# Optimization experiments

Hardware: AMD Instinct MI355X
Metric: run time of the kernel (lower is better)

Reference implementation:

```python
import jax, jax.numpy as jnp
import numpy as np

N, E, F, H, C, G = 100000, 1600000, 128, 4, 32, 64
D = H * C  # 128, per-layer node dim
NEG_SLOPE = 0.2
BN_EPS = 1e-5


def setup_inputs() -> dict:
    key = jax.random.key(0)
    ks = jax.random.split(key, 24)
    inp = {
        "x": jax.random.normal(ks[0], (N, F), jnp.float32),
        "edge_index": jax.random.randint(ks[1], (2, E), 0, N, jnp.int64),
        "batch": jnp.sort(jax.random.randint(ks[2], (N,), 0, G, jnp.int64)),
        # GATConv layer 0: in=F, out=C per head
        "w0": jax.random.normal(ks[3], (F, H * C), jnp.float32) * 0.1,
        "att_src0": jax.random.normal(ks[4], (H, C), jnp.float32) * 0.1,
        "att_dst0": jax.random.normal(ks[5], (H, C), jnp.float32) * 0.1,
        "bias0": jax.random.normal(ks[6], (H * C,), jnp.float32) * 0.1,
        # GATConv layer 1: in=D, out=C per head
        "w1": jax.random.normal(ks[7], (D, H * C), jnp.float32) * 0.1,
        "att_src1": jax.random.normal(ks[8], (H, C), jnp.float32) * 0.1,
        "att_dst1": jax.random.normal(ks[9], (H, C), jnp.float32) * 0.1,
        "bias1": jax.random.normal(ks[10], (H * C,), jnp.float32) * 0.1,
        # BatchNorm (eval mode: running stats)
        "bn_g0": jax.random.normal(ks[11], (D,), jnp.float32) * 0.1 + 1.0,
        "bn_b0": jax.random.normal(ks[12], (D,), jnp.float32) * 0.1,
        "bn_m0": jax.random.normal(ks[13], (D,), jnp.float32) * 0.1,
        "bn_v0": jax.random.uniform(ks[14], (D,), jnp.float32) + 0.5,
        "bn_g1": jax.random.normal(ks[15], (D,), jnp.float32) * 0.1 + 1.0,
        "bn_b1": jax.random.normal(ks[16], (D,), jnp.float32) * 0.1,
        "bn_m1": jax.random.normal(ks[17], (D,), jnp.float32) * 0.1,
        "bn_v1": jax.random.uniform(ks[18], (D,), jnp.float32) + 0.5,
        # head MLP
        "lin1_w": jax.random.normal(ks[19], (D, D // 2), jnp.float32) * 0.1,
        "lin1_b": jax.random.normal(ks[20], (D // 2,), jnp.float32) * 0.1,
        "lin2_w": jax.random.normal(ks[21], (D // 2, 1), jnp.float32) * 0.1,
        "lin2_b": jax.random.normal(ks[22], (1,), jnp.float32) * 0.1,
    }
    return inp


def gat_conv(x, src, dst, w, att_s, att_d, bias):
    """PyG GATConv (concat=True, add_self_loops already in src/dst), eval mode."""
    n = x.shape[0]
    h = (x @ w).reshape(n, H, C)                       # [N,H,C]
    a_s = jnp.sum(h * att_s, axis=-1)                   # [N,H]
    a_d = jnp.sum(h * att_d, axis=-1)                   # [N,H]
    e = jax.nn.leaky_relu(a_s[src] + a_d[dst], NEG_SLOPE)  # [Etot,H]
    m = jax.ops.segment_max(e, dst, num_segments=n)
    m = jax.lax.stop_gradient(jnp.where(jnp.isfinite(m), m, 0.0))
    ex = jnp.exp(e - m[dst])
    denom = jax.ops.segment_sum(ex, dst, num_segments=n)
    alpha = ex / (denom[dst] + 1e-16)                    # segment softmax over dst
    out = jax.ops.segment_sum(h[src] * alpha[:, :, None], dst, num_segments=n)
    return out.reshape(n, H * C) + bias


def bn_eval(x, g, b, m, v):
    return (x - m) * jax.lax.rsqrt(v + BN_EPS) * g + b


def reference(x, edge_index, batch,
              w0, att_src0, att_dst0, bias0,
              w1, att_src1, att_dst1, bias1,
              bn_g0, bn_b0, bn_m0, bn_v0,
              bn_g1, bn_b1, bn_m1, bn_v1,
              lin1_w, lin1_b, lin2_w, lin2_b):
    n = x.shape[0]
    loops = jnp.arange(n, dtype=edge_index.dtype)
    src = jnp.concatenate([edge_index[0], loops])
    dst = jnp.concatenate([edge_index[1], loops])

    h = gat_conv(x, src, dst, w0, att_src0, att_dst0, bias0)
    h = jax.nn.relu(bn_eval(h, bn_g0, bn_b0, bn_m0, bn_v0))
    h = gat_conv(h, src, dst, w1, att_src1, att_dst1, bias1)
    h = jax.nn.relu(bn_eval(h, bn_g1, bn_b1, bn_m1, bn_v1))

    # global mean pool over graphs
    summed = jax.ops.segment_sum(h, batch, num_segments=G)           # [G,D]
    counts = jax.ops.segment_sum(jnp.ones((n,), h.dtype), batch, num_segments=G)
    pooled = summed / jnp.maximum(counts, 1.0)[:, None]

    z = jax.nn.relu(pooled @ lin1_w + lin1_b)
    return z @ lin2_w + lin2_b                                        # [G,1]
```

## Files before the change

### kernel.cpp

```cpp
#include <hip/hip_runtime.h>

#define GG 64
#define STRIDE 10240
#define NBINMAX 256

typedef __attribute__((ext_vector_type(8))) short short8;
typedef __attribute__((ext_vector_type(4))) float f32x4;


__device__ inline unsigned short bf16rne(float f) {
  unsigned int x = __float_as_uint(f);
  unsigned int r = (x + 0x7FFFu + ((x >> 16) & 1u)) >> 16;
  return (unsigned short)r;
}
__device__ inline unsigned int pack2(float a, float b) {
  return (unsigned int)bf16rne(a) | ((unsigned int)bf16rne(b) << 16);
}
__device__ inline float blo(unsigned int v) { return __uint_as_float(v << 16); }
__device__ inline float bhi(unsigned int v) { return __uint_as_float(v & 0xFFFF0000u); }


__global__ __launch_bounds__(256) void init_gcur(int* __restrict__ gcur) {
  gcur[threadIdx.x] = threadIdx.x * STRIDE;
}

__global__ __launch_bounds__(256) void part_p1(const int* __restrict__ ei,
                                               int* __restrict__ gcur,
                                               unsigned int* __restrict__ pairs,
                                               int E, int N) {
  __shared__ int hist[NBINMAX];
  __shared__ int gbase[NBINMAX];
  __shared__ int lcur[NBINMAX];
  int t = threadIdx.x;
  int tot = E + N;
  int base = blockIdx.x * 4096;
  hist[t] = 0;
  __syncthreads();
  int sarr[16], darr[16];
  #pragma unroll
  for (int k = 0; k < 16; ++k) {
    int i = base + k * 256 + t;
    if (i < tot) {
      int s, d;
      if (i < E) { s = ei[i]; d = ei[E + i]; } else { s = i - E; d = s; }
      sarr[k] = s; darr[k] = d;
      atomicAdd(&hist[d >> 9], 1);
    } else darr[k] = -1;
  }
  __syncthreads();
  int c = hist[t];
  gbase[t] = (c > 0) ? atomicAdd(&gcur[t], c) : 0;
  lcur[t] = 0;
  __syncthreads();
  #pragma unroll
  for (int k = 0; k < 16; ++k) {
    int d = darr[k];
    if (d >= 0) {
      int b = d >> 9;
      int p = gbase[b] + atomicAdd(&lcur[b], 1);
      pairs[p] = ((unsigned int)(d & 511) << 17) | (unsigned int)sarr[k];
    }
  }
}


__global__ __launch_bounds__(256) void part_p2(const unsigned int* __restrict__ pairs,
                                               const int* __restrict__ gcur,
                                               int* __restrict__ ssrc,
                                               int* __restrict__ offsets,
                                               int* __restrict__ counts, int N) {
  __shared__ int ncnt[512], ncur[512], excl_s[512];
  __shared__ int wsum[4];
  int b = blockIdx.x;
  int t = threadIdx.x;
  int pb = b * STRIDE;
  int cnt = gcur[b] - pb;
  ncnt[t] = 0; ncnt[t + 256] = 0;
  __syncthreads();
  for (int e = t; e < cnt; e += 256) {
    unsigned int v = pairs[pb + e];
    atomicAdd(&ncnt[v >> 17], 1);
  }
  __syncthreads();
  int c0 = ncnt[2 * t], c1 = ncnt[2 * t + 1];
  int ps = c0 + c1;
  int lane = t & 63, w = t >> 6;
  int x = ps;
  #pragma unroll
  for (int s = 1; s < 64; s <<= 1) { int y = __shfl_up(x, s); if (lane >= s) x += y; }
  if (lane == 63) wsum[w] = x;
  __syncthreads();
  int woff = 0;
  for (int i = 0; i < w; ++i) woff += wsum[i];
  int ep = woff + x - ps;
  excl_s[2 * t]     = ep;
  excl_s[2 * t + 1] = ep + c0;
  __syncthreads();
  int binstart = b << 9;
  for (int i = t; i < 512; i += 256) {
    ncur[i] = excl_s[i];
    int node = binstart + i;
    if (node < N) { offsets[node] = pb + excl_s[i]; counts[node] = ncnt[i]; }
  }
  __syncthreads();
  for (int e = t; e < cnt; e += 256) {
    unsigned int v = pairs[pb + e];
    int dl = v >> 17;
    int p = atomicAdd(&ncur[dl], 1);
    ssrc[pb + p] = (int)(v & 0x1FFFF);
  }
}


__global__ __launch_bounds__(256) void gbounds(const int* __restrict__ batch,
                                               int* __restrict__ gstart, int N) {
  int i = blockIdx.x * 256 + threadIdx.x;
  if (i >= N) return;
  int g = batch[i];
  if (i == 0 || batch[i - 1] != g) gstart[g] = i;
}

__global__ void gfix(const int* __restrict__ gstart, int* __restrict__ go,
                     int* __restrict__ ge, int N) {
  if (threadIdx.x == 0 && blockIdx.x == 0) {
    int nxt = N;
    for (int g = GG - 1; g >= 0; --g) {
      int s = gstart[g];
      if (s < 0) { go[g] = nxt; ge[g] = nxt; }
      else       { go[g] = s;   ge[g] = nxt; nxt = s; }
    }
  }
}


__global__ __launch_bounds__(256) void wprep(const float* __restrict__ w0,
                                             const float* __restrict__ w1,
                                             unsigned short* __restrict__ wt) {
  int idx = blockIdx.x * 256 + threadIdx.x;
  int layer = idx >> 14;
  int e = idx & 16383;
  int k = e >> 7, n = e & 127;
  float v = (layer ? w1 : w0)[e];
  unsigned short hi = bf16rne(v);
  float hif = __uint_as_float((unsigned int)hi << 16);
  unsigned short lo = bf16rne(v - hif);
  unsigned short* basep = wt + layer * 32768;
  basep[n * 128 + k] = hi;
  basep[16384 + n * 128 + k] = lo;
}


__global__ __launch_bounds__(256) void gemm_mfma(
    const float* __restrict__ in, const unsigned short* __restrict__ wtL,
    const float* __restrict__ att_s, const float* __restrict__ att_d,
    unsigned int* __restrict__ h16, float* __restrict__ a_s,
    float* __restrict__ a_d, int N) {
  __shared__ unsigned short xh[128][40], xl[128][40];
  int t = threadIdx.x;
  int bid = blockIdx.x;
  int ch = bid & 1;
  int base = (bid >> 1) * 128;
  int lane = t & 63, w = t >> 6;
  int l15 = lane & 15, lg = lane >> 4;
  int hd = w & 1;
  int n0 = ch * 64 + hd * 32;
  int rh = w >> 1;

  f32x4 zero4 = {0.f, 0.f, 0.f, 0.f};
  f32x4 acc[4][2];
  #pragma unroll
  for (int rt = 0; rt < 4; ++rt) { acc[rt][0] = zero4; acc[rt][1] = zero4; }

  int sr = t >> 1;
  int sc = (t & 1) * 16;
  int gr = base + sr;
  int rc = gr < N ? gr : (N - 1);
  const float* xp = &in[(size_t)rc * 128 + sc];

  const unsigned short* wh0 = &wtL[(size_t)(n0 + l15) * 128];
  const unsigned short* wh1 = &wtL[(size_t)(n0 + 16 + l15) * 128];

  float4 u0 = *(const float4*)(xp + 0);
  float4 u1 = *(const float4*)(xp + 4);
  float4 u2 = *(const float4*)(xp + 8);
  float4 u3 = *(const float4*)(xp + 12);
  short8 cbh0 = *(const short8*)(wh0 + lg * 8);
  short8 cbh1 = *(const short8*)(wh1 + lg * 8);
  short8 cbl0 = *(const short8*)(wh0 + 16384 + lg * 8);
  short8 cbl1 = *(const short8*)(wh1 + 16384 + lg * 8);

  #pragma unroll
  for (int kt = 0; kt < 4; ++kt) {
    if (kt) __syncthreads();
    {
      float4 uu[4] = {u0, u1, u2, u3};
      #pragma unroll
      for (int q = 0; q < 4; ++q) {
        float4 u = uu[q];
        unsigned int b0 = __float_as_uint(u.x), b1 = __float_as_uint(u.y);
        unsigned int b2 = __float_as_uint(u.z), b3 = __float_as_uint(u.w);
        *(unsigned int*)&xh[sr][sc + q * 4]     = __builtin_amdgcn_perm(b1, b0, 0x07060302u);
        *(unsigned int*)&xh[sr][sc + q * 4 + 2] = __builtin_amdgcn_perm(b3, b2, 0x07060302u);
        float r0 = u.x - __uint_as_float(b0 & 0xFFFF0000u);
        float r1 = u.y - __uint_as_float(b1 & 0xFFFF0000u);
        float r2 = u.z - __uint_as_float(b2 & 0xFFFF0000u);
        float r3 = u.w - __uint_as_float(b3 & 0xFFFF0000u);
        *(unsigned int*)&xl[sr][sc + q * 4] =
            __builtin_amdgcn_perm(__float_as_uint(r1), __float_as_uint(r0), 0x07060302u);
        *(unsigned int*)&xl[sr][sc + q * 4 + 2] =
            __builtin_amdgcn_perm(__float_as_uint(r3), __float_as_uint(r2), 0x07060302u);
      }
    }
    __syncthreads();
    float4 v0 = u0, v1 = u1, v2 = u2, v3 = u3;
    short8 nbh0 = cbh0, nbh1 = cbh1, nbl0 = cbl0, nbl1 = cbl1;
    if (kt < 3) {
      int k1 = (kt + 1) * 32;
      v0 = *(const float4*)(xp + k1);
      v1 = *(const float4*)(xp + k1 + 4);
      v2 = *(const float4*)(xp + k1 + 8);
      v3 = *(const float4*)(xp + k1 + 12);
      nbh0 = *(const short8*)(wh0 + k1 + lg * 8);
      nbh1 = *(const short8*)(wh1 + k1 + lg * 8);
      nbl0 = *(const short8*)(wh0 + 16384 + k1 + lg * 8);
      nbl1 = *(const short8*)(wh1 + 16384 + k1 + lg * 8);
    }
    #pragma unroll
    for (int rt = 0; rt < 4; ++rt) {
      int row = rh * 64 + rt * 16 + l15;
      short8 fah = *(const short8*)&xh[row][lg * 8];
      short8 fal = *(const short8*)&xl[row][lg * 8];
      acc[rt][0] = __builtin_amdgcn_mfma_f32_16x16x32_bf16(fah, cbh0, acc[rt][0], 0, 0, 0);
      acc[rt][1] = __builtin_amdgcn_mfma_f32_16x16x32_bf16(fah, cbh1, acc[rt][1], 0, 0, 0);
      acc[rt][0] = __builtin_amdgcn_mfma_f32_16x16x32_bf16(fal, cbh0, acc[rt][0], 0, 0, 0);
      acc[rt][1] = __builtin_amdgcn_mfma_f32_16x16x32_bf16(fal, cbh1, acc[rt][1], 0, 0, 0);
      acc[rt][0] = __builtin_amdgcn_mfma_f32_16x16x32_bf16(fah, cbl0, acc[rt][0], 0, 0, 0);
      acc[rt][1] = __builtin_amdgcn_mfma_f32_16x16x32_bf16(fah, cbl1, acc[rt][1], 0, 0, 0);
    }
    u0 = v0; u1 = v1; u2 = v2; u3 = v3;
    cbh0 = nbh0; cbh1 = nbh1; cbl0 = nbl0; cbl1 = nbl1;
  }

  int headg = ch * 2 + hd;
  float as0 = att_s[n0 + l15], as1 = att_s[n0 + 16 + l15];
  float ad0 = att_d[n0 + l15], ad1 = att_d[n0 + 16 + l15];
  #pragma unroll
  for (int rt = 0; rt < 4; ++rt) {
    float ps[4], pd[4];
    #pragma unroll
    for (int q = 0; q < 4; ++q) {
      float c0v = acc[rt][0][q], c1v = acc[rt][1][q];
      float p0 = __shfl_xor(c0v, 1), p1 = __shfl_xor(c1v, 1);
      int row = base + rh * 64 + rt * 16 + lg * 4 + q;
      if (!(l15 & 1) && row < N) {
        h16[(size_t)row * 64 + (n0 + l15) / 2]      = pack2(c0v, p0);
        h16[(size_t)row * 64 + (n0 + 16 + l15) / 2] = pack2(c1v, p1);
      }
      ps[q] = c0v * as0 + c1v * as1;
      pd[q] = c0v * ad0 + c1v * ad1;
    }
    #pragma unroll
    for (int m = 1; m <= 8; m <<= 1) {
      #pragma unroll
      for (int q = 0; q < 4; ++q) { ps[q] += __shfl_xor(ps[q], m); pd[q] += __shfl_xor(pd[q], m); }
    }
    if (l15 == 0) {
      #pragma unroll
      for (int q = 0; q < 4; ++q) {
        int row = base + rh * 64 + rt * 16 + lg * 4 + q;
        if (row < N) { a_s[row * 4 + headg] = ps[q]; a_d[row * 4 + headg] = pd[q]; }
      }
    }
  }
}


#define ACCP(EX, V0, V1)                                                       \
  { float2 ex2 = make_float2(EX, EX);                                          \
    acc2[0] += ex2 * make_float2(blo(V0.x), bhi(V0.x));                        \
    acc2[1] += ex2 * make_float2(blo(V0.y), bhi(V0.y));                        \
    acc2[2] += ex2 * make_float2(blo(V0.z), bhi(V0.z));                        \
    acc2[3] += ex2 * make_float2(blo(V0.w), bhi(V0.w));                        \
    acc2[4] += ex2 * make_float2(blo(V1.x), bhi(V1.x));                        \
    acc2[5] += ex2 * make_float2(blo(V1.y), bhi(V1.y));                        \
    acc2[6] += ex2 * make_float2(blo(V1.z), bhi(V1.z));                        \
    acc2[7] += ex2 * make_float2(blo(V1.w), bhi(V1.w)); }

__global__ __launch_bounds__(256) void gat_aggregate(
    const unsigned int* __restrict__ h16, const float* __restrict__ a_s, const float* __restrict__ a_d,
    const int* __restrict__ offsets, const int* __restrict__ counts, const int* __restrict__ ssrc,
    const float* __restrict__ bias,
    const float* __restrict__ bn_g, const float* __restrict__ bn_b,
    const float* __restrict__ bn_m, const float* __restrict__ bn_v,
    float* __restrict__ out, int N) {
  __shared__ float part[4][8][132];
  int wv = threadIdx.x >> 6;
  int lane = threadIdx.x & 63;
  int wid = blockIdx.x * 4 + wv;
  if (wid >= N) return;
  int off = offsets[wid], cnt = counts[wid];
  int eg = lane >> 3;
  int j  = lane & 7;
  int hh = j >> 1;
  float ad = a_d[wid * 4 + hh];

  float2 acc2[8] = {};
  float den = 0.f;

  int sA = ssrc[off + (eg < cnt ? eg : 0)];
  int iB0 = eg + 8;
  int sB = ssrc[off + (iB0 < cnt ? iB0 : 0)];
  float asA = a_s[sA * 4 + hh];
  float asB = a_s[sB * 4 + hh];

  for (int i = eg; i < cnt; i += 16) {
    const uint4* hpA = (const uint4*)(h16 + (size_t)sA * 64 + j * 8);
    uint4 va0 = hpA[0], va1 = hpA[1];
    const uint4* hpB = (const uint4*)(h16 + (size_t)sB * 64 + j * 8);
    uint4 vb0 = hpB[0], vb1 = hpB[1];
    int in0 = i + 16, in1 = i + 24;
    int snA = ssrc[off + (in0 < cnt ? in0 : 0)];
    int snB = ssrc[off + (in1 < cnt ? in1 : 0)];
    float anA = a_s[snA * 4 + hh];
    float anB = a_s[snB * 4 + hh];
    float eA = asA + ad; eA = eA > 0.f ? eA : 0.2f * eA;
    float exA = __expf(eA);
    float eB = asB + ad; eB = eB > 0.f ? eB : 0.2f * eB;
    float exB = ((i + 8) < cnt) ? __expf(eB) : 0.f;
    den += exA + exB;
    ACCP(exA, va0, va1)
    ACCP(exB, vb0, vb1)
    sA = snA; sB = snB; asA = anA; asB = anB;
  }

  den += __shfl_xor(den, 8);
  den += __shfl_xor(den, 16);
  den += __shfl_xor(den, 32);
  den = __shfl(den, (lane >> 4) * 2);

  float* pw = &part[wv][eg][j * 16];
  *(float4*)(pw + 0)  = make_float4(acc2[0].x, acc2[0].y, acc2[1].x, acc2[1].y);
  *(float4*)(pw + 4)  = make_float4(acc2[2].x, acc2[2].y, acc2[3].x, acc2[3].y);
  *(float4*)(pw + 8)  = make_float4(acc2[4].x, acc2[4].y, acc2[5].x, acc2[5].y);
  *(float4*)(pw + 12) = make_float4(acc2[6].x, acc2[6].y, acc2[7].x, acc2[7].y);
  asm volatile("s_waitcnt lgkmcnt(0)" ::: "memory");

  int d = lane * 2;
  float r0 = 0.f, r1 = 0.f;
  #pragma unroll
  for (int g = 0; g < 8; ++g) {
    float2 v = *(const float2*)(&part[wv][g][d]);
    r0 += v.x; r1 += v.y;
  }

  float inv = 1.f / (den + 1e-16f);
  float2 bi = *(const float2*)(&bias[d]);
  float2 g2 = *(const float2*)(&bn_g[d]);
  float2 b2 = *(const float2*)(&bn_b[d]);
  float2 m2 = *(const float2*)(&bn_m[d]);
  float2 v2 = *(const float2*)(&bn_v[d]);
  float o0 = r0 * inv + bi.x;
  float o1 = r1 * inv + bi.y;
  o0 = fmaxf((o0 - m2.x) * (g2.x * rsqrtf(v2.x + 1e-5f)) + b2.x, 0.f);
  o1 = fmaxf((o1 - m2.y) * (g2.y * rsqrtf(v2.y + 1e-5f)) + b2.y, 0.f);
  *(float2*)(&out[(size_t)wid * 128 + d]) = make_float2(o0, o1);
}


#define POOLP 8

__global__ __launch_bounds__(256) void pool_kernel(const float* __restrict__ y,
                                                   const int* __restrict__ go,
                                                   const int* __restrict__ ge,
                                                   float* __restrict__ pooled) {
  int g = blockIdx.x / POOLP, p = blockIdx.x % POOLP;
  int s = go[g], e = ge[g];
  int len = e - s;
  int q0 = s + (len * p) / POOLP, q1 = s + (len * (p + 1)) / POOLP;
  int t = threadIdx.x;
  int d = t & 127, half = t >> 7;
  float acc = 0.f;
  for (int i = q0 + half; i < q1; i += 2) acc += y[(size_t)i * 128 + d];
  __shared__ float red[256];
  red[t] = acc;
  __syncthreads();
  if (half == 0) atomicAdd(&pooled[g * 128 + d], red[d] + red[d + 128]);
}

__global__ __launch_bounds__(64) void mlp_kernel(const float* __restrict__ pooled,
                                                 const int* __restrict__ go,
                                                 const int* __restrict__ ge,
                                                 const float* __restrict__ w1,
                                                 const float* __restrict__ b1,
                                                 const float* __restrict__ w2,
                                                 const float* __restrict__ b2,
                                                 float* __restrict__ out) {
  int g = blockIdx.x, j = threadIdx.x;
  int cnt = ge[g] - go[g];
  float inv = 1.f / (float)(cnt > 1 ? cnt : 1);
  float z = b1[j];
  for (int k = 0; k < 128; ++k) z += pooled[g * 128 + k] * inv * w1[k * 64 + j];
  z = fmaxf(z, 0.f);
  float v = z * w2[j];
  #pragma unroll
  for (int m = 1; m < 64; m <<= 1) v += __shfl_xor(v, m);
  if (j == 0) out[g] = v + b2[0];
}


extern "C" void kernel_launch(void* const* d_in, const int* in_sizes, int n_in,
                              void* d_out, int out_size, void* d_ws, size_t ws_size,
                              hipStream_t stream) {
  const float* x     = (const float*)d_in[0];
  const int*   ei    = (const int*)d_in[1];
  const int*   batch = (const int*)d_in[2];
  const float* w0    = (const float*)d_in[3];
  const float* atts0 = (const float*)d_in[4];
  const float* attd0 = (const float*)d_in[5];
  const float* bias0 = (const float*)d_in[6];
  const float* w1    = (const float*)d_in[7];
  const float* atts1 = (const float*)d_in[8];
  const float* attd1 = (const float*)d_in[9];
  const float* bias1 = (const float*)d_in[10];
  const float* bng0  = (const float*)d_in[11];
  const float* bnb0  = (const float*)d_in[12];
  const float* bnm0  = (const float*)d_in[13];
  const float* bnv0  = (const float*)d_in[14];
  const float* bng1  = (const float*)d_in[15];
  const float* bnb1  = (const float*)d_in[16];
  const float* bnm1  = (const float*)d_in[17];
  const float* bnv1  = (const float*)d_in[18];
  const float* l1w   = (const float*)d_in[19];
  const float* l1b   = (const float*)d_in[20];
  const float* l2w   = (const float*)d_in[21];
  const float* l2b   = (const float*)d_in[22];

  int N = in_sizes[2];
  int E = in_sizes[1] / 2;
  int tot = E + N;
  int NBIN = (N + 511) / 512;

  char* p = (char*)d_ws;
  unsigned int* h16 = (unsigned int*)p; p += (size_t)N * 128 * 2;
  float* y_buf  = (float*)p; p += (size_t)N * 128 * 4;
  float* a_s    = (float*)p; p += (size_t)N * 4 * 4;
  float* a_d    = (float*)p; p += (size_t)N * 4 * 4;
  int* counts   = (int*)p;   p += (size_t)N * 4;
  int* offsets  = (int*)p;   p += (size_t)N * 4;
  int* ssrc     = (int*)p;   p += (size_t)NBINMAX * STRIDE * 4;
  int* gcur     = (int*)p;   p += NBINMAX * 4;
  int* gstart   = (int*)p;   p += 64 * 4;
  int* go       = (int*)p;   p += 64 * 4;
  int* ge       = (int*)p;   p += 64 * 4;
  float* pooled = (float*)p; p += 64 * 128 * 4;
  unsigned short* wt = (unsigned short*)p; p += 2 * 32768 * 2;
  unsigned int* pairs = (unsigned int*)y_buf;

  hipMemsetAsync(gstart, 0xFF, 64 * 4, stream);
  hipMemsetAsync(pooled, 0, 64 * 128 * 4, stream);

  int bN = (N + 255) / 256;
  int bW = (N + 3) / 4;
  int bG2 = 2 * ((N + 127) / 128);

  init_gcur<<<1, 256, 0, stream>>>(gcur);
  part_p1<<<(tot + 4095) / 4096, 256, 0, stream>>>(ei, gcur, pairs, E, N);
  part_p2<<<NBIN, 256, 0, stream>>>(pairs, gcur, ssrc, offsets, counts, N);
  gbounds<<<bN, 256, 0, stream>>>(batch, gstart, N);
  gfix<<<1, 64, 0, stream>>>(gstart, go, ge, N);
  wprep<<<128, 256, 0, stream>>>(w0, w1, wt);

  gemm_mfma<<<bG2, 256, 0, stream>>>(x, wt, atts0, attd0, h16, a_s, a_d, N);
  gat_aggregate<<<bW, 256, 0, stream>>>(h16, a_s, a_d, offsets, counts, ssrc,
                                        bias0, bng0, bnb0, bnm0, bnv0, y_buf, N);
  gemm_mfma<<<bG2, 256, 0, stream>>>(y_buf, wt + 32768, atts1, attd1, h16, a_s, a_d, N);
  gat_aggregate<<<bW, 256, 0, stream>>>(h16, a_s, a_d, offsets, counts, ssrc,
                                        bias1, bng1, bnb1, bnm1, bnv1, y_buf, N);
  pool_kernel<<<GG * POOLP, 256, 0, stream>>>(y_buf, go, ge, pooled);
  mlp_kernel<<<GG, 64, 0, stream>>>(pooled, go, ge, l1w, l1b, l2w, l2b, (float*)d_out);
}
```

Before: 327.8 us.

## Load GEMM A fragments directly from global, fold init_gcur into wprep, parallelize gfix

The GEMM kernel no longer stages the input tile through LDS. Each lane loads its MFMA A-fragment straight from global memory and splits it into bf16 hi/lo in registers, which removes both __syncthreads barriers per k-step and the LDS traffic. In exchange, the software prefetch of the next k-slice is gone, and each row is now read with 32-byte per-lane loads rather than cooperatively. Separately, init_gcur is merged into wprep to save a launch, and gfix's serial loop becomes a wave-wide suffix-min scan.

```diff
diff --git a/kernel.cpp b/kernel.cpp
--- a/kernel.cpp
+++ b/kernel.cpp
@@ -19,10 +19,6 @@
 __device__ inline float blo(unsigned int v) { return __uint_as_float(v << 16); }
 __device__ inline float bhi(unsigned int v) { return __uint_as_float(v & 0xFFFF0000u); }
 
-
-__global__ __launch_bounds__(256) void init_gcur(int* __restrict__ gcur) {
-  gcur[threadIdx.x] = threadIdx.x * STRIDE;
-}
 
 __global__ __launch_bounds__(256) void part_p1(const int* __restrict__ ei,
                                                int* __restrict__ gcur,
@@ -120,22 +116,31 @@
   if (i == 0 || batch[i - 1] != g) gstart[g] = i;
 }
 
-__global__ void gfix(const int* __restrict__ gstart, int* __restrict__ go,
-                     int* __restrict__ ge, int N) {
-  if (threadIdx.x == 0 && blockIdx.x == 0) {
-    int nxt = N;
-    for (int g = GG - 1; g >= 0; --g) {
-      int s = gstart[g];
-      if (s < 0) { go[g] = nxt; ge[g] = nxt; }
-      else       { go[g] = s;   ge[g] = nxt; nxt = s; }
-    }
-  }
+__global__ __launch_bounds__(64) void gfix(const int* __restrict__ gstart,
+                                           int* __restrict__ go,
+                                           int* __restrict__ ge, int N) {
+  int g = threadIdx.x;
+  int s = gstart[g];
+  int v = (s < 0) ? 0x7FFFFFFF : s;
+  int suf = v;
+  #pragma unroll
+  for (int off = 1; off < 64; off <<= 1) {
+    int x = __shfl_down(suf, off);
+    if (g + off < 64) suf = min(suf, x);
+  }
+  int nxt = __shfl_down(suf, 1);
+  if (g == 63) nxt = 0x7FFFFFFF;
+  int e = nxt == 0x7FFFFFFF ? N : nxt;
+  if (s < 0) { go[g] = e; ge[g] = e; }
+  else       { go[g] = s; ge[g] = e; }
 }
 
 
 __global__ __launch_bounds__(256) void wprep(const float* __restrict__ w0,
                                              const float* __restrict__ w1,
-                                             unsigned short* __restrict__ wt) {
+                                             unsigned short* __restrict__ wt,
+                                             int* __restrict__ gcur) {
+  if (blockIdx.x == 0) gcur[threadIdx.x] = threadIdx.x * STRIDE;
   int idx = blockIdx.x * 256 + threadIdx.x;
   int layer = idx >> 14;
   int e = idx & 16383;
@@ -155,7 +160,6 @@
     const float* __restrict__ att_s, const float* __restrict__ att_d,
     unsigned int* __restrict__ h16, float* __restrict__ a_s,
     float* __restrict__ a_d, int N) {
-  __shared__ unsigned short xh[128][40], xl[128][40];
   int t = threadIdx.x;
   int bid = blockIdx.x;
   int ch = bid & 1;
@@ -171,65 +175,50 @@
   #pragma unroll
   for (int rt = 0; rt < 4; ++rt) { acc[rt][0] = zero4; acc[rt][1] = zero4; }
 
-  int sr = t >> 1;
-  int sc = (t & 1) * 16;
-  int gr = base + sr;
-  int rc = gr < N ? gr : (N - 1);
-  const float* xp = &in[(size_t)rc * 128 + sc];
-
-  const unsigned short* wh0 = &wtL[(size_t)(n0 + l15) * 128];
-  const unsigned short* wh1 = &wtL[(size_t)(n0 + 16 + l15) * 128];
-
-  float4 u0 = *(const float4*)(xp + 0);
-  float4 u1 = *(const float4*)(xp + 4);
-  float4 u2 = *(const float4*)(xp + 8);
-  float4 u3 = *(const float4*)(xp + 12);
-  short8 cbh0 = *(const short8*)(wh0 + lg * 8);
-  short8 cbh1 = *(const short8*)(wh1 + lg * 8);
-  short8 cbl0 = *(const short8*)(wh0 + 16384 + lg * 8);
-  short8 cbl1 = *(const short8*)(wh1 + 16384 + lg * 8);
+  const float* ap[4];
+  #pragma unroll
+  for (int rt = 0; rt < 4; ++rt) {
+    int row = base + rh * 64 + rt * 16 + l15;
+    int rc = row < N ? row : (N - 1);
+    ap[rt] = &in[(size_t)rc * 128 + lg * 8];
+  }
+  const unsigned short* wh0 = &wtL[(size_t)(n0 + l15) * 128 + lg * 8];
+  const unsigned short* wh1 = &wtL[(size_t)(n0 + 16 + l15) * 128 + lg * 8];
 
   #pragma unroll
   for (int kt = 0; kt < 4; ++kt) {
-    if (kt) __syncthreads();
-    {
-      float4 uu[4] = {u0, u1, u2, u3};
-      #pragma unroll
-      for (int q = 0; q < 4; ++q) {
-        float4 u = uu[q];
-        unsigned int b0 = __float_as_uint(u.x), b1 = __float_as_uint(u.y);
-        unsigned int b2 = __float_as_uint(u.z), b3 = __float_as_uint(u.w);
-        *(unsigned int*)&xh[sr][sc + q * 4]     = __builtin_amdgcn_perm(b1, b0, 0x07060302u);
-        *(unsigned int*)&xh[sr][sc + q * 4 + 2] = __builtin_amdgcn_perm(b3, b2, 0x07060302u);
-        float r0 = u.x - __uint_as_float(b0 & 0xFFFF0000u);
-        float r1 = u.y - __uint_as_float(b1 & 0xFFFF0000u);
-        float r2 = u.z - __uint_as_float(b2 & 0xFFFF0000u);
-        float r3 = u.w - __uint_as_float(b3 & 0xFFFF0000u);
-        *(unsigned int*)&xl[sr][sc + q * 4] =
-            __builtin_amdgcn_perm(__float_as_uint(r1), __float_as_uint(r0), 0x07060302u);
-        *(unsigned int*)&xl[sr][sc + q * 4 + 2] =
-            __builtin_amdgcn_perm(__float_as_uint(r3), __float_as_uint(r2), 0x07060302u);
-      }
-    }
-    __syncthreads();
-    float4 v0 = u0, v1 = u1, v2 = u2, v3 = u3;
-    short8 nbh0 = cbh0, nbh1 = cbh1, nbl0 = cbl0, nbl1 = cbl1;
-    if (kt < 3) {
-      int k1 = (kt + 1) * 32;
-      v0 = *(const float4*)(xp + k1);
-      v1 = *(const float4*)(xp + k1 + 4);
-      v2 = *(const float4*)(xp + k1 + 8);
-      v3 = *(const float4*)(xp + k1 + 12);
-      nbh0 = *(const short8*)(wh0 + k1 + lg * 8);
-      nbh1 = *(const short8*)(wh1 + k1 + lg * 8);
-      nbl0 = *(const short8*)(wh0 + 16384 + k1 + lg * 8);
-      nbl1 = *(const short8*)(wh1 + 16384 + k1 + lg * 8);
-    }
+    int k0 = kt * 32;
+    short8 cbh0 = *(const short8*)(wh0 + k0);
+    short8 cbh1 = *(const short8*)(wh1 + k0);
+    short8 cbl0 = *(const short8*)(wh0 + 16384 + k0);
+    short8 cbl1 = *(const short8*)(wh1 + 16384 + k0);
     #pragma unroll
     for (int rt = 0; rt < 4; ++rt) {
-      int row = rh * 64 + rt * 16 + l15;
-      short8 fah = *(const short8*)&xh[row][lg * 8];
-      short8 fal = *(const short8*)&xl[row][lg * 8];
+      float4 a0 = *(const float4*)(ap[rt] + k0);
+      float4 a1 = *(const float4*)(ap[rt] + k0 + 4);
+      unsigned int b0 = __float_as_uint(a0.x), b1 = __float_as_uint(a0.y);
+      unsigned int b2 = __float_as_uint(a0.z), b3 = __float_as_uint(a0.w);
+      unsigned int b4 = __float_as_uint(a1.x), b5 = __float_as_uint(a1.y);
+      unsigned int b6 = __float_as_uint(a1.z), b7 = __float_as_uint(a1.w);
+      unsigned int fh[4], fl[4];
+      fh[0] = __builtin_amdgcn_perm(b1, b0, 0x07060302u);
+      fh[1] = __builtin_amdgcn_perm(b3, b2, 0x07060302u);
+      fh[2] = __builtin_amdgcn_perm(b5, b4, 0x07060302u);
+      fh[3] = __builtin_amdgcn_perm(b7, b6, 0x07060302u);
+      float r0 = a0.x - __uint_as_float(b0 & 0xFFFF0000u);
+      float r1 = a0.y - __uint_as_float(b1 & 0xFFFF0000u);
+      float r2 = a0.z - __uint_as_float(b2 & 0xFFFF0000u);
+      float r3 = a0.w - __uint_as_float(b3 & 0xFFFF0000u);
+      float r4 = a1.x - __uint_as_float(b4 & 0xFFFF0000u);
+      float r5 = a1.y - __uint_as_float(b5 & 0xFFFF0000u);
+      float r6 = a1.z - __uint_as_float(b6 & 0xFFFF0000u);
+      float r7 = a1.w - __uint_as_float(b7 & 0xFFFF0000u);
+      fl[0] = __builtin_amdgcn_perm(__float_as_uint(r1), __float_as_uint(r0), 0x07060302u);
+      fl[1] = __builtin_amdgcn_perm(__float_as_uint(r3), __float_as_uint(r2), 0x07060302u);
+      fl[2] = __builtin_amdgcn_perm(__float_as_uint(r5), __float_as_uint(r4), 0x07060302u);
+      fl[3] = __builtin_amdgcn_perm(__float_as_uint(r7), __float_as_uint(r6), 0x07060302u);
+      short8 fah = *(short8*)fh;
+      short8 fal = *(short8*)fl;
       acc[rt][0] = __builtin_amdgcn_mfma_f32_16x16x32_bf16(fah, cbh0, acc[rt][0], 0, 0, 0);
       acc[rt][1] = __builtin_amdgcn_mfma_f32_16x16x32_bf16(fah, cbh1, acc[rt][1], 0, 0, 0);
       acc[rt][0] = __builtin_amdgcn_mfma_f32_16x16x32_bf16(fal, cbh0, acc[rt][0], 0, 0, 0);
@@ -237,8 +226,6 @@
       acc[rt][0] = __builtin_amdgcn_mfma_f32_16x16x32_bf16(fah, cbl0, acc[rt][0], 0, 0, 0);
       acc[rt][1] = __builtin_amdgcn_mfma_f32_16x16x32_bf16(fah, cbl1, acc[rt][1], 0, 0, 0);
     }
-    u0 = v0; u1 = v1; u2 = v2; u3 = v3;
-    cbh0 = nbh0; cbh1 = nbh1; cbl0 = nbl0; cbl1 = nbl1;
   }
 
   int headg = ch * 2 + hd;
@@ -463,12 +450,11 @@
   int bW = (N + 3) / 4;
   int bG2 = 2 * ((N + 127) / 128);
 
-  init_gcur<<<1, 256, 0, stream>>>(gcur);
+  wprep<<<128, 256, 0, stream>>>(w0, w1, wt, gcur);
   part_p1<<<(tot + 4095) / 4096, 256, 0, stream>>>(ei, gcur, pairs, E, N);
   part_p2<<<NBIN, 256, 0, stream>>>(pairs, gcur, ssrc, offsets, counts, N);
   gbounds<<<bN, 256, 0, stream>>>(batch, gstart, N);
   gfix<<<1, 64, 0, stream>>>(gstart, go, ge, N);
-  wprep<<<128, 256, 0, stream>>>(w0, w1, wt);
 
   gemm_mfma<<<bG2, 256, 0, stream>>>(x, wt, atts0, attd0, h16, a_s, a_d, N);
   gat_aggregate<<<bW, 256, 0, stream>>>(h16, a_s, a_d, offsets, counts, ssrc,
```

After: 354.9 us. 1.08x slower.
